# Optimization experiments

Measured on AMD Instinct MI355X. Metric: run time of the kernel, lower is better.

## Reference

```python
import jax, jax.numpy as jnp
import numpy as np

INPUT_SIZE = 1000
EMB = 1024          # 2**ceil(log2(input_size))
NQ = 10             # log2(EMB)
NL = 3              # n_qlayers (hardcoded in module)
B = 4096


def _rot(phi, theta, omega):
    # PennyLane qml.Rot(phi, theta, omega) = RZ(omega) RY(theta) RZ(phi)
    c = jnp.cos(theta * 0.5).astype(jnp.complex64)
    s = jnp.sin(theta * 0.5).astype(jnp.complex64)
    ea = jnp.exp(-0.5j * (phi + omega))   # e^{-i(phi+omega)/2}
    eb = jnp.exp(0.5j * (phi - omega))    # e^{ i(phi-omega)/2}
    row0 = jnp.stack([ea * c, -eb * s])
    row1 = jnp.stack([jnp.conj(eb) * s, jnp.conj(ea) * c])
    return jnp.stack([row0, row1])        # [2, 2] complex64


def _apply_1q(psi, U, q):
    # psi: [B] + [2]*NQ ; contract qubit axis q+1 with U
    psi = jnp.tensordot(psi, U, axes=[[q + 1], [1]])
    return jnp.moveaxis(psi, -1, q + 1)


def _apply_cnot(psi, c, t):
    c_ax, t_ax = c + 1, t + 1
    psi0 = jax.lax.index_in_dim(psi, 0, axis=c_ax, keepdims=False)
    psi1 = jax.lax.index_in_dim(psi, 1, axis=c_ax, keepdims=False)
    f_ax = t_ax - 1 if t_ax > c_ax else t_ax
    psi1 = jnp.flip(psi1, axis=f_ax)      # X on target when control=1
    return jnp.stack([psi0, psi1], axis=c_ax)


def _circuit(x, w):
    # AmplitudeEmbedding(normalize=True) + StronglyEntanglingLayers + probs
    norm = jnp.sqrt(jnp.sum(x * x, axis=1, keepdims=True))
    psi = (x / norm).astype(jnp.complex64)
    b = psi.shape[0]
    psi = psi.reshape((b,) + (2,) * NQ)   # wire 0 = most-significant bit
    for l in range(NL):
        for q in range(NQ):
            psi = _apply_1q(psi, _rot(w[l, q, 0], w[l, q, 1], w[l, q, 2]), q)
        r = l % (NQ - 1) + 1              # default SEL ranges
        for q in range(NQ):
            psi = _apply_cnot(psi, q, (q + r) % NQ)
    return (psi.real ** 2 + psi.imag ** 2).reshape(b, -1)  # probs [B, 2**NQ]


def setup_inputs() -> dict:
    key = jax.random.key(0)
    ks = jax.random.split(key, 12)
    d = {
        'inputs': jax.random.normal(ks[0], (B, INPUT_SIZE), jnp.float32),
        'weightsEnc': 0.1 * jax.random.normal(ks[1], (NL, NQ, 3), jnp.float32),
        'weightsDec': 0.1 * jax.random.normal(ks[2], (NL, NQ, 3), jnp.float32),
        'W0': jax.random.normal(ks[3], (INPUT_SIZE, EMB), jnp.float32) / np.sqrt(INPUT_SIZE),
        'b0': jnp.zeros((EMB,), jnp.float32),
        'W1': jax.random.normal(ks[4], (EMB, 2 * EMB), jnp.float32) / np.sqrt(EMB),
        'b1': jnp.zeros((2 * EMB,), jnp.float32),
        'W2': jax.random.normal(ks[5], (2 * EMB, EMB), jnp.float32) / np.sqrt(2 * EMB),
        'b2': jnp.zeros((EMB,), jnp.float32),
        'W3': jax.random.normal(ks[6], (EMB, INPUT_SIZE), jnp.float32) / np.sqrt(EMB),
        'b3': jnp.zeros((INPUT_SIZE,), jnp.float32),
    }
    return d


def reference(inputs, weightsEnc, weightsDec, W0, b0, W1, b1, W2, b2, W3, b3):
    x = inputs @ W0 + b0                 # Dense(embedding_dim)
    x = _circuit(x, weightsEnc)          # encoder qnode (vmapped over batch)
    x = x @ W1 + b1                      # Dense(2*embedding_dim)
    x = x @ W2 + b2                      # Dense(embedding_dim)
    x = _circuit(x, weightsDec)          # decoder qnode
    x = x @ W3 + b3                      # Dense(input_size)
    x = jnp.abs(x)
    return x / jnp.sum(x, axis=1, keepdims=True)
```

## Files before the change

kernel.cpp:

```cpp
#include <hip/hip_runtime.h>
#include <math.h>


#define B_SZ 4096
#define EMB 1024
#define NQ 10
#define NL 3

typedef __bf16 bf16x8 __attribute__((ext_vector_type(8)));
typedef float f32x4 __attribute__((ext_vector_type(4)));
typedef unsigned short u16x8 __attribute__((ext_vector_type(8)));

__device__ __forceinline__ unsigned short f2bf_rne(float f) {
    unsigned int u = __float_as_uint(f);
    u += 0x7FFFu + ((u >> 16) & 1u);
    return (unsigned short)(u >> 16);
}
__device__ __forceinline__ float bf2f(unsigned short h) {
    return __uint_as_float(((unsigned int)h) << 16);
}
__device__ __forceinline__ float lane_bcast(float v, int l) {
    return __uint_as_float(__builtin_amdgcn_readlane(__float_as_uint(v), l));
}

template<int M>
__device__ __forceinline__ float lane_xor(float v) {
    if constexpr (M == 1)
        return __uint_as_float(__builtin_amdgcn_mov_dpp(__float_as_uint(v), 0xB1, 0xF, 0xF, true));
    else if constexpr (M == 2)
        return __uint_as_float(__builtin_amdgcn_mov_dpp(__float_as_uint(v), 0x4E, 0xF, 0xF, true));
    else if constexpr (M == 8)
        return __uint_as_float(__builtin_amdgcn_mov_dpp(__float_as_uint(v), 0x128, 0xF, 0xF, true));
    else if constexpr (M == 4)
        return __uint_as_float(__builtin_amdgcn_ds_swizzle(__float_as_uint(v), 0x101F));
    else if constexpr (M == 16)
        return __uint_as_float(__builtin_amdgcn_ds_swizzle(__float_as_uint(v), 0x401F));
    else
        return __shfl_xor(v, 32, 64);
}

__device__ __forceinline__ void gll16(const void* g, void* l) {
    __builtin_amdgcn_global_load_lds(
        (const __attribute__((address_space(1))) void*)g,
        (__attribute__((address_space(3))) void*)l, 16, 0, 0);
}

#define GBM 128
#define GBN 128
#define GBK 32

__global__ __launch_bounds__(512) void gemm3_mfma(
    const unsigned short* __restrict__ Ah, const unsigned short* __restrict__ Al,
    const unsigned short* __restrict__ Bh, const unsigned short* __restrict__ Bl,
    const float* __restrict__ bias, float* __restrict__ C,
    int Kp, int Np, int Ksplit, size_t zStride)
{
    __shared__ __align__(16) char lds[32768];
    char* ldsAh = lds;
    char* ldsAl = lds + 8192;
    char* ldsBh = lds + 16384;
    char* ldsBl = lds + 24576;

    const int tid = threadIdx.x;
    const int lane = tid & 63;
    const int wv = tid >> 6;
    const int wm = wv >> 1;
    const int wn = wv & 1;
    const int blockRow = blockIdx.y * GBM;
    const int blockCol = blockIdx.x * GBN;
    const int z = blockIdx.z;

    const int srow = tid >> 2;
    const int skel = (tid & 3) * 8;
    const size_t aOff = ((size_t)(blockRow + srow) * Kp + skel + (size_t)z * Ksplit) * 2;
    const size_t bOff = ((size_t)(blockCol + srow) * Kp + skel + (size_t)z * Ksplit) * 2;
    const char* aHp = (const char*)Ah + aOff;
    const char* aLp = (const char*)Al + aOff;
    const char* bHp = (const char*)Bh + bOff;
    const char* bLp = (const char*)Bl + bOff;
    const int stageOff = wv * 1024;

    f32x4 acc[2][4];
    #pragma unroll
    for (int i = 0; i < 2; ++i)
        #pragma unroll
        for (int j = 0; j < 4; ++j)
            #pragma unroll
            for (int r = 0; r < 4; ++r) acc[i][j][r] = 0.f;

    const int kq = (lane >> 4) * 16;
    int aFragOff[2], bFragOff[4];
    #pragma unroll
    for (int i = 0; i < 2; ++i) aFragOff[i] = (wm * 32 + i * 16 + (lane & 15)) * 64 + kq;
    #pragma unroll
    for (int j = 0; j < 4; ++j) bFragOff[j] = (wn * 64 + j * 16 + (lane & 15)) * 64 + kq;

    const int nsteps = Ksplit / GBK;
    for (int s = 0; s < nsteps; ++s) {
        const size_t kb = (size_t)s * GBK * 2;
        gll16(aHp + kb, ldsAh + stageOff);
        gll16(aLp + kb, ldsAl + stageOff);
        gll16(bHp + kb, ldsBh + stageOff);
        gll16(bLp + kb, ldsBl + stageOff);
        __syncthreads();

        bf16x8 ah[2], al[2], bh[4], bl[4];
        #pragma unroll
        for (int i = 0; i < 2; ++i) {
            ah[i] = *(const bf16x8*)(ldsAh + aFragOff[i]);
            al[i] = *(const bf16x8*)(ldsAl + aFragOff[i]);
        }
        #pragma unroll
        for (int j = 0; j < 4; ++j) {
            bh[j] = *(const bf16x8*)(ldsBh + bFragOff[j]);
            bl[j] = *(const bf16x8*)(ldsBl + bFragOff[j]);
        }
        #pragma unroll
        for (int j = 0; j < 4; ++j)
            #pragma unroll
            for (int i = 0; i < 2; ++i) {
                acc[i][j] = __builtin_amdgcn_mfma_f32_16x16x32_bf16(al[i], bh[j], acc[i][j], 0, 0, 0);
                acc[i][j] = __builtin_amdgcn_mfma_f32_16x16x32_bf16(ah[i], bl[j], acc[i][j], 0, 0, 0);
                acc[i][j] = __builtin_amdgcn_mfma_f32_16x16x32_bf16(ah[i], bh[j], acc[i][j], 0, 0, 0);
            }
        __syncthreads();
    }

    float* Cz = C + (size_t)z * zStride;
    const bool addB = (z == 0) && (bias != nullptr);
    const int rquad = (lane >> 4) * 4;
    const int cidx = lane & 15;
    #pragma unroll
    for (int i = 0; i < 2; ++i)
        #pragma unroll
        for (int j = 0; j < 4; ++j) {
            #pragma unroll
            for (int r = 0; r < 4; ++r) {
                int row = blockRow + wm * 32 + i * 16 + rquad + r;
                int col = blockCol + wn * 64 + j * 16 + cidx;
                float v = acc[i][j][r];
                if (addB) v += bias[col];
                Cz[(size_t)row * Np + col] = v;
            }
        }
}

__device__ __forceinline__ void tsplit_block(
    const float* __restrict__ W, unsigned short* __restrict__ H, unsigned short* __restrict__ L,
    int K, int N, int Kp, int bx, int by, int tid)
{
    __shared__ float tile[32][33];
    const int tx = tid & 31, ty = tid >> 5;
    const int k0 = bx * 32, n0 = by * 32;
    #pragma unroll
    for (int i = 0; i < 4; ++i) {
        int k = k0 + ty + i * 8, n = n0 + tx;
        tile[ty + i * 8][tx] = (k < K && n < N) ? W[(size_t)k * N + n] : 0.f;
    }
    __syncthreads();
    #pragma unroll
    for (int i = 0; i < 4; ++i) {
        int n = n0 + ty + i * 8, k = k0 + tx;
        float v = tile[tx][ty + i * 8];
        size_t o = (size_t)n * Kp + k;
        unsigned short h = f2bf_rne(v);
        H[o] = h;
        L[o] = f2bf_rne(v - bf2f(h));
    }
}

__global__ __launch_bounds__(256) void prep_weights_kernel(
    const float* __restrict__ W0, unsigned short* __restrict__ Bt0h, unsigned short* __restrict__ Bt0l,
    const float* __restrict__ W2, unsigned short* __restrict__ Bt2h, unsigned short* __restrict__ Bt2l,
    const float* __restrict__ W3, unsigned short* __restrict__ Bt3h, unsigned short* __restrict__ Bt3l,
    const float* __restrict__ W1, unsigned short* __restrict__ W1h, unsigned short* __restrict__ W1l)
{
    const int bid = blockIdx.x;
    const int tid = threadIdx.x;
    if (bid < 1024) {
        tsplit_block(W0, Bt0h, Bt0l, 1000, 1024, 1024, bid & 31, bid >> 5, tid);
    } else if (bid < 3072) {
        int b = bid - 1024;
        tsplit_block(W2, Bt2h, Bt2l, 2048, 1024, 2048, b & 63, b >> 6, tid);
    } else if (bid < 4096) {
        int b = bid - 3072;
        tsplit_block(W3, Bt3h, Bt3l, 1024, 1000, 1024, b & 31, b >> 5, tid);
    } else {
        int r = bid - 4096;
        for (int c = tid; c < 2048; c += 256) {
            float v = W1[(size_t)r * 2048 + c];
            unsigned short h = f2bf_rne(v);
            size_t o = (size_t)r * 2048 + c;
            W1h[o] = h;
            W1l[o] = f2bf_rne(v - bf2f(h));
        }
    }
}

__global__ __launch_bounds__(256) void prep_misc_kernel(
    const float* __restrict__ b1, const float* __restrict__ W2, const float* __restrict__ b2,
    float* __restrict__ b12,
    const float* __restrict__ b3, float* __restrict__ b3p,
    const float* __restrict__ wEnc, const float* __restrict__ wDec, float* __restrict__ G)
{
    __shared__ float red[4][64];
    const int bid = blockIdx.x;
    const int tid = threadIdx.x;
    if (bid < 16) {
        const int tx = tid & 63, ty = tid >> 6;
        const int n = bid * 64 + tx;
        float s = 0.f;
        for (int j = ty * 512; j < (ty + 1) * 512; ++j)
            s += b1[j] * W2[(size_t)j * 1024 + n];
        red[ty][tx] = s;
        __syncthreads();
        if (ty == 0) b12[n] = red[0][tx] + red[1][tx] + red[2][tx] + red[3][tx] + b2[n];
    } else if (bid < 20) {
        int i = (bid - 16) * 256 + tid;
        b3p[i] = (i < 1000) ? b3[i] : 0.f;
    } else {
        int g = tid;
        if (g < 60) {
            const float* w = (g < 30) ? (wEnc + g * 3) : (wDec + (g - 30) * 3);
            float* o = G + ((g < 30) ? g : (g - 30 + 64)) * 8;
            float phi = w[0], th = w[1], om = w[2];
            float ch = cosf(0.5f * th), sh = sinf(0.5f * th);
            float ap = 0.5f * (phi + om), am = 0.5f * (phi - om);
            float cap = cosf(ap), sap = sinf(ap);
            float cam = cosf(am), sam = sinf(am);
            o[0] =  cap * ch; o[1] = -sap * ch;
            o[2] = -cam * sh; o[3] = -sam * sh;
            o[4] =  cam * sh; o[5] = -sam * sh;
            o[6] =  cap * ch; o[7] =  sap * ch;
        }
    }
}

__global__ __launch_bounds__(256) void tsplit8_kernel(
    const float* __restrict__ P, unsigned short* __restrict__ H, unsigned short* __restrict__ L)
{
    __shared__ float tile[32][33];
    const int tid = threadIdx.x;
    const int tx = tid & 31, ty = tid >> 5;
    const int k0 = blockIdx.x * 32, n0 = blockIdx.y * 32;
    #pragma unroll
    for (int i = 0; i < 4; ++i) {
        int k = k0 + ty + i * 8, n = n0 + tx;
        size_t o = (size_t)k * 1024 + n;
        float s = 0.f;
        #pragma unroll
        for (int zz = 0; zz < 8; ++zz) s += P[o + ((size_t)zz << 20)];
        tile[ty + i * 8][tx] = s;
    }
    __syncthreads();
    #pragma unroll
    for (int i = 0; i < 4; ++i) {
        int n = n0 + ty + i * 8, k = k0 + tx;
        float v = tile[tx][ty + i * 8];
        size_t o = (size_t)n * 1024 + k;
        unsigned short h = f2bf_rne(v);
        H[o] = h;
        L[o] = f2bf_rne(v - bf2f(h));
    }
}

__global__ __launch_bounds__(256) void split_rows_kernel(
    const float* __restrict__ X, unsigned short* __restrict__ H, unsigned short* __restrict__ L,
    int C, int Cp)
{
    const int r = blockIdx.x;
    for (int c = threadIdx.x; c < Cp; c += 256) {
        float v = (c < C) ? X[(size_t)r * C + c] : 0.f;
        unsigned short h = f2bf_rne(v);
        size_t o = (size_t)r * Cp + c;
        H[o] = h;
        L[o] = f2bf_rne(v - bf2f(h));
    }
}


template<int GATE, int Q>
__device__ __forceinline__ void apply_rot(float (&xr)[16], float (&xi)[16],
                                          const float (&tbl)[8], int lane)
{
    float are = lane_bcast(tbl[0], GATE), aim = lane_bcast(tbl[1], GATE);
    float bre = lane_bcast(tbl[2], GATE), bim = lane_bcast(tbl[3], GATE);
    float cre = lane_bcast(tbl[4], GATE), cim = lane_bcast(tbl[5], GATE);
    float dre = lane_bcast(tbl[6], GATE), dim_ = lane_bcast(tbl[7], GATE);
    constexpr int S = 1 << (9 - Q);
    if constexpr (S < 16) {
        #pragma unroll
        for (int p = 0; p < 8; ++p) {
            int r0 = (p / S) * (2 * S) + (p % S);
            int r1 = r0 + S;
            float x0r = xr[r0], x0i = xi[r0], x1r = xr[r1], x1i = xi[r1];
            xr[r0] = are * x0r - aim * x0i + bre * x1r - bim * x1i;
            xi[r0] = are * x0i + aim * x0r + bre * x1i + bim * x1r;
            xr[r1] = cre * x0r - cim * x0i + dre * x1r - dim_ * x1i;
            xi[r1] = cre * x0i + cim * x0r + dre * x1i + dim_ * x1r;
        }
    } else {
        constexpr int M = S >> 4;
        bool bit = (lane & M) != 0;
        float pre = bit ? dre : are, pim = bit ? dim_ : aim;
        float qre = bit ? cre : bre, qim = bit ? cim : bim;
        #pragma unroll
        for (int r = 0; r < 16; ++r) {
            float ore = lane_xor<M>(xr[r]);
            float oim = lane_xor<M>(xi[r]);
            float nr = pre * xr[r] - pim * xi[r] + qre * ore - qim * oim;
            float ni = pre * xi[r] + pim * xr[r] + qre * oim + qim * ore;
            xr[r] = nr; xi[r] = ni;
        }
    }
}

template<int C, int T>
__device__ __forceinline__ void apply_cnot(float (&xr)[16], float (&xi)[16], int lane)
{
    constexpr int SC = 1 << (9 - C), ST = 1 << (9 - T);
    if constexpr (SC < 16 && ST < 16) {
        #pragma unroll
        for (int r = 0; r < 16; ++r) {
            if ((r & SC) && !(r & ST)) {
                int j = r | ST;
                float t;
                t = xr[r]; xr[r] = xr[j]; xr[j] = t;
                t = xi[r]; xi[r] = xi[j]; xi[j] = t;
            }
        }
    } else if constexpr (SC < 16) {
        constexpr int MT = ST >> 4;
        #pragma unroll
        for (int r = 0; r < 16; ++r) {
            if (r & SC) {
                xr[r] = lane_xor<MT>(xr[r]);
                xi[r] = lane_xor<MT>(xi[r]);
            }
        }
    } else if constexpr (ST < 16) {
        constexpr int MC = SC >> 4;
        bool bit = (lane & MC) != 0;
        #pragma unroll
        for (int r = 0; r < 16; ++r) {
            if (!(r & ST)) {
                int j = r | ST;
                float a0 = xr[r], a1 = xr[j];
                xr[r] = bit ? a1 : a0;  xr[j] = bit ? a0 : a1;
                float b0 = xi[r], b1 = xi[j];
                xi[r] = bit ? b1 : b0;  xi[j] = bit ? b0 : b1;
            }
        }
    } else {
        constexpr int MC = SC >> 4, MT = ST >> 4;
        bool bit = (lane & MC) != 0;
        #pragma unroll
        for (int r = 0; r < 16; ++r) {
            float o = lane_xor<MT>(xr[r]);
            xr[r] = bit ? o : xr[r];
            float oi = lane_xor<MT>(xi[r]);
            xi[r] = bit ? oi : xi[r];
        }
    }
}

template<int L, int Q>
__device__ __forceinline__ void rots(float (&xr)[16], float (&xi)[16],
                                     const float (&tbl)[8], int lane) {
    apply_rot<L * 10 + Q, Q>(xr, xi, tbl, lane);
    if constexpr (Q < 9) rots<L, Q + 1>(xr, xi, tbl, lane);
}
template<int L, int Q>
__device__ __forceinline__ void cnots(float (&xr)[16], float (&xi)[16], int lane) {
    constexpr int R = (L % 9) + 1;
    apply_cnot<Q, (Q + R) % 10>(xr, xi, lane);
    if constexpr (Q < 9) cnots<L, Q + 1>(xr, xi, lane);
}

__global__ __launch_bounds__(256, 4) void circuit_reg_kernel(
    const float* __restrict__ X0, const float* __restrict__ X1,
    unsigned short* __restrict__ Ph, unsigned short* __restrict__ Pl,
    const float* __restrict__ G)
{
    const int lane = threadIdx.x & 63;
    const int item = blockIdx.x * 4 + (threadIdx.x >> 6);
    const size_t base = (size_t)item * 1024 + lane * 16;

    float tbl[8];
    {
        const float4* gp = (const float4*)(G + lane * 8);
        float4 t0 = gp[0], t1 = gp[1];
        tbl[0] = t0.x; tbl[1] = t0.y; tbl[2] = t0.z; tbl[3] = t0.w;
        tbl[4] = t1.x; tbl[5] = t1.y; tbl[6] = t1.z; tbl[7] = t1.w;
    }

    float xr[16], xi[16];
    const float4* xb0 = (const float4*)(X0 + base);
    const float4* xb1 = (const float4*)(X1 + base);
    #pragma unroll
    for (int v = 0; v < 4; ++v) {
        float4 f = xb0[v], g = xb1[v];
        xr[v * 4 + 0] = f.x + g.x; xr[v * 4 + 1] = f.y + g.y;
        xr[v * 4 + 2] = f.z + g.z; xr[v * 4 + 3] = f.w + g.w;
    }
    #pragma unroll
    for (int r = 0; r < 16; ++r) xi[r] = 0.f;

    float nrm = 0.f;
    #pragma unroll
    for (int r = 0; r < 16; ++r) nrm += xr[r] * xr[r];
    nrm += lane_xor<1>(nrm);
    nrm += lane_xor<2>(nrm);
    nrm += lane_xor<4>(nrm);
    nrm += lane_xor<8>(nrm);
    nrm += lane_xor<16>(nrm);
    nrm += lane_xor<32>(nrm);
    float inv = 1.0f / sqrtf(nrm);
    #pragma unroll
    for (int r = 0; r < 16; ++r) xr[r] *= inv;

    rots<0, 0>(xr, xi, tbl, lane);  cnots<0, 0>(xr, xi, lane);
    rots<1, 0>(xr, xi, tbl, lane);  cnots<1, 0>(xr, xi, lane);
    rots<2, 0>(xr, xi, tbl, lane);  cnots<2, 0>(xr, xi, lane);

    u16x8 h[2], lo[2];
    #pragma unroll
    for (int r = 0; r < 16; ++r) {
        float p = xr[r] * xr[r] + xi[r] * xi[r];
        unsigned short hh = f2bf_rne(p);
        h[r >> 3][r & 7] = hh;
        lo[r >> 3][r & 7] = f2bf_rne(p - bf2f(hh));
    }
    *(u16x8*)(Ph + base) = h[0];
    *(u16x8*)(Ph + base + 8) = h[1];
    *(u16x8*)(Pl + base) = lo[0];
    *(u16x8*)(Pl + base + 8) = lo[1];
}

__global__ __launch_bounds__(256) void absnorm_kernel(
    const float* __restrict__ X0, const float* __restrict__ X1,
    float* __restrict__ out, int N, int stride)
{
    __shared__ float red[4];
    const int row = blockIdx.x;
    const int tid = threadIdx.x;
    const float* x0 = X0 + (size_t)row * stride;
    const float* x1 = X1 + (size_t)row * stride;

    float s = 0.f;
    for (int i = tid; i < N; i += 256) s += fabsf(x0[i] + x1[i]);
    #pragma unroll
    for (int off = 32; off > 0; off >>= 1) s += __shfl_down(s, off);
    if ((tid & 63) == 0) red[tid >> 6] = s;
    __syncthreads();
    float inv = 1.0f / (red[0] + red[1] + red[2] + red[3]);
    for (int i = tid; i < N; i += 256)
        out[(size_t)row * N + i] = fabsf(x0[i] + x1[i]) * inv;
}

extern "C" void kernel_launch(void* const* d_in, const int* in_sizes, int n_in,
                              void* d_out, int out_size, void* d_ws, size_t ws_size,
                              hipStream_t stream)
{
    const float* inputs = (const float*)d_in[0];
    const float* wEnc   = (const float*)d_in[1];
    const float* wDec   = (const float*)d_in[2];
    const float* W0     = (const float*)d_in[3];
    const float* b0     = (const float*)d_in[4];
    const float* W1     = (const float*)d_in[5];
    const float* b1     = (const float*)d_in[6];
    const float* W2     = (const float*)d_in[7];
    const float* b2     = (const float*)d_in[8];
    const float* W3     = (const float*)d_in[9];
    const float* b3     = (const float*)d_in[10];
    float* out = (float*)d_out;

    char* w = (char*)d_ws;
    auto alloc = [&](size_t bytes) { char* p = w; w += (bytes + 255) & ~(size_t)255; return p; };

    unsigned short* Bt0h  = (unsigned short*)alloc((size_t)1024 * 1024 * 2);
    unsigned short* Bt0l  = (unsigned short*)alloc((size_t)1024 * 1024 * 2);
    unsigned short* Bt2h  = (unsigned short*)alloc((size_t)1024 * 2048 * 2);
    unsigned short* Bt2l  = (unsigned short*)alloc((size_t)1024 * 2048 * 2);
    unsigned short* Bt3h  = (unsigned short*)alloc((size_t)1024 * 1024 * 2);
    unsigned short* Bt3l  = (unsigned short*)alloc((size_t)1024 * 1024 * 2);
    unsigned short* Bt12h = (unsigned short*)alloc((size_t)1024 * 1024 * 2);
    unsigned short* Bt12l = (unsigned short*)alloc((size_t)1024 * 1024 * 2);
    unsigned short* W1h   = (unsigned short*)alloc((size_t)1024 * 2048 * 2);
    unsigned short* W1l   = (unsigned short*)alloc((size_t)1024 * 2048 * 2);
    float*          b3p   = (float*)alloc(1024 * 4);
    float*          b12   = (float*)alloc(1024 * 4);
    float*          G     = (float*)alloc(2 * 512 * 4);
    unsigned short* Ah    = (unsigned short*)alloc((size_t)B_SZ * 1024 * 2);
    unsigned short* Al    = (unsigned short*)alloc((size_t)B_SZ * 1024 * 2);
    unsigned short* ph    = (unsigned short*)alloc((size_t)B_SZ * 1024 * 2);
    unsigned short* pl    = (unsigned short*)alloc((size_t)B_SZ * 1024 * 2);
    float*          P     = (float*)alloc((size_t)2 * B_SZ * 1024 * 4);
    float* P12 = P;
    const size_t ZS = (size_t)B_SZ * 1024;

    dim3 blk256(256);

    prep_weights_kernel<<<5120, blk256, 0, stream>>>(
        W0, Bt0h, Bt0l, W2, Bt2h, Bt2l, W3, Bt3h, Bt3l, W1, W1h, W1l);
    prep_misc_kernel<<<21, blk256, 0, stream>>>(b1, W2, b2, b12, b3, b3p, wEnc, wDec, G);
    split_rows_kernel<<<B_SZ, blk256, 0, stream>>>(inputs, Ah, Al, 1000, 1024);

    gemm3_mfma<<<dim3(8, 8, 8), 512, 0, stream>>>(
        W1h, W1l, Bt2h, Bt2l, nullptr, P12, 2048, 1024, 256, (size_t)1 << 20);
    tsplit8_kernel<<<dim3(32, 32), blk256, 0, stream>>>(P12, Bt12h, Bt12l);

    gemm3_mfma<<<dim3(8, 32, 2), 512, 0, stream>>>(
        Ah, Al, Bt0h, Bt0l, b0, P, 1024, 1024, 512, ZS);
    circuit_reg_kernel<<<B_SZ / 4, blk256, 0, stream>>>(P, P + ZS, ph, pl, G);
    gemm3_mfma<<<dim3(8, 32, 2), 512, 0, stream>>>(
        ph, pl, Bt12h, Bt12l, b12, P, 1024, 1024, 512, ZS);
    circuit_reg_kernel<<<B_SZ / 4, blk256, 0, stream>>>(P, P + ZS, ph, pl, G + 512);
    gemm3_mfma<<<dim3(8, 32, 2), 512, 0, stream>>>(
        ph, pl, Bt3h, Bt3l, b3p, P, 1024, 1024, 512, ZS);
    absnorm_kernel<<<B_SZ, blk256, 0, stream>>>(P, P + ZS, out, 1000, 1024);
}
```

Before: 413.4 us.

## Load GEMM fragments directly from global, merge prep kernels, vectorize absnorm

The split-bf16 MFMA GEMM no longer stages tiles through LDS with global_load_lds and barriers. Each lane now loads its bf16x8 fragments straight from global memory, with an unrolled k-loop and a launch-bounds occupancy hint. Separately, the three preprocessing kernels are folded into one launch, and absnorm is rewritten to use float4 loads that keep values in registers instead of reading the inputs twice. The aim is to remove barrier stalls and launch overhead. The risk is redundant global and L2 traffic, since each fragment is fetched by several waves instead of being shared through LDS.

Measured after the change: 610.8 us. 1.48x slower.

```diff
diff --git a/kernel.cpp b/kernel.cpp
--- a/kernel.cpp
+++ b/kernel.cpp
@@ -39,28 +39,15 @@
         return __shfl_xor(v, 32, 64);
 }
 
-__device__ __forceinline__ void gll16(const void* g, void* l) {
-    __builtin_amdgcn_global_load_lds(
-        (const __attribute__((address_space(1))) void*)g,
-        (__attribute__((address_space(3))) void*)l, 16, 0, 0);
-}
-
 #define GBM 128
 #define GBN 128
-#define GBK 32
-
-__global__ __launch_bounds__(512) void gemm3_mfma(
+
+__global__ __launch_bounds__(512, 4) void gemm3_mfma(
     const unsigned short* __restrict__ Ah, const unsigned short* __restrict__ Al,
     const unsigned short* __restrict__ Bh, const unsigned short* __restrict__ Bl,
     const float* __restrict__ bias, float* __restrict__ C,
     int Kp, int Np, int Ksplit, size_t zStride)
 {
-    __shared__ __align__(16) char lds[32768];
-    char* ldsAh = lds;
-    char* ldsAl = lds + 8192;
-    char* ldsBh = lds + 16384;
-    char* ldsBl = lds + 24576;
-
     const int tid = threadIdx.x;
     const int lane = tid & 63;
     const int wv = tid >> 6;
@@ -70,15 +57,16 @@
     const int blockCol = blockIdx.x * GBN;
     const int z = blockIdx.z;
 
-    const int srow = tid >> 2;
-    const int skel = (tid & 3) * 8;
-    const size_t aOff = ((size_t)(blockRow + srow) * Kp + skel + (size_t)z * Ksplit) * 2;
-    const size_t bOff = ((size_t)(blockCol + srow) * Kp + skel + (size_t)z * Ksplit) * 2;
-    const char* aHp = (const char*)Ah + aOff;
-    const char* aLp = (const char*)Al + aOff;
-    const char* bHp = (const char*)Bh + bOff;
-    const char* bLp = (const char*)Bl + bOff;
-    const int stageOff = wv * 1024;
+    const int kq = (lane >> 4) * 8;
+    const int m0 = blockRow + wm * 32 + (lane & 15);
+    const int n0 = blockCol + wn * 64 + (lane & 15);
+    const size_t kbase = (size_t)z * Ksplit + kq;
+
+    size_t aOff[2], bOff[4];
+    #pragma unroll
+    for (int i = 0; i < 2; ++i) aOff[i] = (size_t)(m0 + i * 16) * Kp + kbase;
+    #pragma unroll
+    for (int j = 0; j < 4; ++j) bOff[j] = (size_t)(n0 + j * 16) * Kp + kbase;
 
     f32x4 acc[2][4];
     #pragma unroll
@@ -88,32 +76,20 @@
             #pragma unroll
             for (int r = 0; r < 4; ++r) acc[i][j][r] = 0.f;
 
-    const int kq = (lane >> 4) * 16;
-    int aFragOff[2], bFragOff[4];
-    #pragma unroll
-    for (int i = 0; i < 2; ++i) aFragOff[i] = (wm * 32 + i * 16 + (lane & 15)) * 64 + kq;
-    #pragma unroll
-    for (int j = 0; j < 4; ++j) bFragOff[j] = (wn * 64 + j * 16 + (lane & 15)) * 64 + kq;
-
-    const int nsteps = Ksplit / GBK;
+    const int nsteps = Ksplit / 32;
+    #pragma unroll 4
     for (int s = 0; s < nsteps; ++s) {
-        const size_t kb = (size_t)s * GBK * 2;
-        gll16(aHp + kb, ldsAh + stageOff);
-        gll16(aLp + kb, ldsAl + stageOff);
-        gll16(bHp + kb, ldsBh + stageOff);
-        gll16(bLp + kb, ldsBl + stageOff);
-        __syncthreads();
-
+        const size_t kk = (size_t)s * 32;
         bf16x8 ah[2], al[2], bh[4], bl[4];
         #pragma unroll
         for (int i = 0; i < 2; ++i) {
-            ah[i] = *(const bf16x8*)(ldsAh + aFragOff[i]);
-            al[i] = *(const bf16x8*)(ldsAl + aFragOff[i]);
+            ah[i] = *(const bf16x8*)(Ah + aOff[i] + kk);
+            al[i] = *(const bf16x8*)(Al + aOff[i] + kk);
         }
         #pragma unroll
         for (int j = 0; j < 4; ++j) {
-            bh[j] = *(const bf16x8*)(ldsBh + bFragOff[j]);
-            bl[j] = *(const bf16x8*)(ldsBl + bFragOff[j]);
+            bh[j] = *(const bf16x8*)(Bh + bOff[j] + kk);
+            bl[j] = *(const bf16x8*)(Bl + bOff[j] + kk);
         }
         #pragma unroll
         for (int j = 0; j < 4; ++j)
@@ -123,7 +99,6 @@
                 acc[i][j] = __builtin_amdgcn_mfma_f32_16x16x32_bf16(ah[i], bl[j], acc[i][j], 0, 0, 0);
                 acc[i][j] = __builtin_amdgcn_mfma_f32_16x16x32_bf16(ah[i], bh[j], acc[i][j], 0, 0, 0);
             }
-        __syncthreads();
     }
 
     float* Cz = C + (size_t)z * zStride;
@@ -169,11 +144,15 @@
     }
 }
 
-__global__ __launch_bounds__(256) void prep_weights_kernel(
+__global__ __launch_bounds__(256) void prep_all_kernel(
     const float* __restrict__ W0, unsigned short* __restrict__ Bt0h, unsigned short* __restrict__ Bt0l,
     const float* __restrict__ W2, unsigned short* __restrict__ Bt2h, unsigned short* __restrict__ Bt2l,
     const float* __restrict__ W3, unsigned short* __restrict__ Bt3h, unsigned short* __restrict__ Bt3l,
-    const float* __restrict__ W1, unsigned short* __restrict__ W1h, unsigned short* __restrict__ W1l)
+    const float* __restrict__ W1, unsigned short* __restrict__ W1h, unsigned short* __restrict__ W1l,
+    const float* __restrict__ X, unsigned short* __restrict__ Ah, unsigned short* __restrict__ Al,
+    const float* __restrict__ b1, const float* __restrict__ b2, float* __restrict__ b12,
+    const float* __restrict__ b3, float* __restrict__ b3p,
+    const float* __restrict__ wEnc, const float* __restrict__ wDec, float* __restrict__ G)
 {
     const int bid = blockIdx.x;
     const int tid = threadIdx.x;
@@ -185,7 +164,7 @@
     } else if (bid < 4096) {
         int b = bid - 3072;
         tsplit_block(W3, Bt3h, Bt3l, 1024, 1000, 1024, b & 31, b >> 5, tid);
-    } else {
+    } else if (bid < 5120) {
         int r = bid - 4096;
         for (int c = tid; c < 2048; c += 256) {
             float v = W1[(size_t)r * 2048 + c];
@@ -194,29 +173,27 @@
             W1h[o] = h;
             W1l[o] = f2bf_rne(v - bf2f(h));
         }
-    }
-}
-
-__global__ __launch_bounds__(256) void prep_misc_kernel(
-    const float* __restrict__ b1, const float* __restrict__ W2, const float* __restrict__ b2,
-    float* __restrict__ b12,
-    const float* __restrict__ b3, float* __restrict__ b3p,
-    const float* __restrict__ wEnc, const float* __restrict__ wDec, float* __restrict__ G)
-{
-    __shared__ float red[4][64];
-    const int bid = blockIdx.x;
-    const int tid = threadIdx.x;
-    if (bid < 16) {
+    } else if (bid < 9216) {
+        int r = bid - 5120;
+        for (int c = tid; c < 1024; c += 256) {
+            float v = (c < 1000) ? X[(size_t)r * 1000 + c] : 0.f;
+            unsigned short h = f2bf_rne(v);
+            size_t o = (size_t)r * 1024 + c;
+            Ah[o] = h;
+            Al[o] = f2bf_rne(v - bf2f(h));
+        }
+    } else if (bid < 9232) {
+        __shared__ float red[4][64];
         const int tx = tid & 63, ty = tid >> 6;
-        const int n = bid * 64 + tx;
+        const int n = (bid - 9216) * 64 + tx;
         float s = 0.f;
         for (int j = ty * 512; j < (ty + 1) * 512; ++j)
             s += b1[j] * W2[(size_t)j * 1024 + n];
         red[ty][tx] = s;
         __syncthreads();
         if (ty == 0) b12[n] = red[0][tx] + red[1][tx] + red[2][tx] + red[3][tx] + b2[n];
-    } else if (bid < 20) {
-        int i = (bid - 16) * 256 + tid;
+    } else if (bid < 9236) {
+        int i = (bid - 9232) * 256 + tid;
         b3p[i] = (i < 1000) ? b3[i] : 0.f;
     } else {
         int g = tid;
@@ -264,20 +241,6 @@
     }
 }
 
-__global__ __launch_bounds__(256) void split_rows_kernel(
-    const float* __restrict__ X, unsigned short* __restrict__ H, unsigned short* __restrict__ L,
-    int C, int Cp)
-{
-    const int r = blockIdx.x;
-    for (int c = threadIdx.x; c < Cp; c += 256) {
-        float v = (c < C) ? X[(size_t)r * C + c] : 0.f;
-        unsigned short h = f2bf_rne(v);
-        size_t o = (size_t)r * Cp + c;
-        H[o] = h;
-        L[o] = f2bf_rne(v - bf2f(h));
-    }
-}
-
 
 template<int GATE, int Q>
 __device__ __forceinline__ void apply_rot(float (&xr)[16], float (&xi)[16],
@@ -438,24 +401,29 @@
 }
 
 __global__ __launch_bounds__(256) void absnorm_kernel(
-    const float* __restrict__ X0, const float* __restrict__ X1,
-    float* __restrict__ out, int N, int stride)
+    const float* __restrict__ P, size_t ZS, float* __restrict__ out, int N)
 {
     __shared__ float red[4];
     const int row = blockIdx.x;
     const int tid = threadIdx.x;
-    const float* x0 = X0 + (size_t)row * stride;
-    const float* x1 = X1 + (size_t)row * stride;
-
+    const size_t rb = (size_t)row * 1024 + tid * 4;
+
+    float4 a = *(const float4*)(P + rb);
+    float4 b = *(const float4*)(P + ZS + rb);
+    float x[4] = { a.x + b.x, a.y + b.y, a.z + b.z, a.w + b.w };
+
+    const int c0 = tid * 4;
     float s = 0.f;
-    for (int i = tid; i < N; i += 256) s += fabsf(x0[i] + x1[i]);
+    #pragma unroll
+    for (int j = 0; j < 4; ++j) if (c0 + j < N) s += fabsf(x[j]);
     #pragma unroll
     for (int off = 32; off > 0; off >>= 1) s += __shfl_down(s, off);
     if ((tid & 63) == 0) red[tid >> 6] = s;
     __syncthreads();
     float inv = 1.0f / (red[0] + red[1] + red[2] + red[3]);
-    for (int i = tid; i < N; i += 256)
-        out[(size_t)row * N + i] = fabsf(x0[i] + x1[i]) * inv;
+    #pragma unroll
+    for (int j = 0; j < 4; ++j)
+        if (c0 + j < N) out[(size_t)row * N + c0 + j] = fabsf(x[j]) * inv;
 }
 
 extern "C" void kernel_launch(void* const* d_in, const int* in_sizes, int n_in,
@@ -501,10 +469,9 @@
 
     dim3 blk256(256);
 
-    prep_weights_kernel<<<5120, blk256, 0, stream>>>(
-        W0, Bt0h, Bt0l, W2, Bt2h, Bt2l, W3, Bt3h, Bt3l, W1, W1h, W1l);
-    prep_misc_kernel<<<21, blk256, 0, stream>>>(b1, W2, b2, b12, b3, b3p, wEnc, wDec, G);
-    split_rows_kernel<<<B_SZ, blk256, 0, stream>>>(inputs, Ah, Al, 1000, 1024);
+    prep_all_kernel<<<9237, blk256, 0, stream>>>(
+        W0, Bt0h, Bt0l, W2, Bt2h, Bt2l, W3, Bt3h, Bt3l, W1, W1h, W1l,
+        inputs, Ah, Al, b1, b2, b12, b3, b3p, wEnc, wDec, G);
 
     gemm3_mfma<<<dim3(8, 8, 8), 512, 0, stream>>>(
         W1h, W1l, Bt2h, Bt2l, nullptr, P12, 2048, 1024, 256, (size_t)1 << 20);
@@ -518,5 +485,5 @@
     circuit_reg_kernel<<<B_SZ / 4, blk256, 0, stream>>>(P, P + ZS, ph, pl, G + 512);
     gemm3_mfma<<<dim3(8, 32, 2), 512, 0, stream>>>(
         ph, pl, Bt3h, Bt3l, b3p, P, 1024, 1024, 512, ZS);
-    absnorm_kernel<<<B_SZ, blk256, 0, stream>>>(P, P + ZS, out, 1000, 1024);
-}
+    absnorm_kernel<<<B_SZ, blk256, 0, stream>>>(P, ZS, out, 1000);
+}
```
